# Performance work log

Measured on AMD Instinct MI355X. Metric: run time of the kernel, lower is better.

The kernel has to match this reference:

```python
import jax, jax.numpy as jnp
import numpy as np

B = 1_000_000  # batch size
A = 40         # number of CelebA face attributes
GAMMA = 2.0
EPS = 1e-12


def setup_inputs() -> dict:
    key = jax.random.key(0)
    k1, k2, k3 = jax.random.split(key, 3)
    inputs = jax.random.uniform(k1, (B, A), dtype=jnp.float32)  # probabilities
    targets = jax.random.randint(k2, (A, B), 0, 2, dtype=jnp.int32)  # binary labels, attr-first layout
    attr_loss_weight = jax.random.uniform(k3, (A,), dtype=jnp.float32) + 0.5  # positive per-attr weights
    return {"inputs": inputs, "targets": targets, "attr_loss_weight": attr_loss_weight}


def reference(inputs, targets, attr_loss_weight):
    # inputs: [B, A] probabilities; targets: [A, B] binary labels
    t = targets.T.astype(inputs.dtype)                      # [B, A]
    p = jnp.clip(inputs, EPS, 1.0 - EPS)
    bce = -(t * jnp.log(p) + (1.0 - t) * jnp.log1p(-p))     # elementwise BCE
    w = attr_loss_weight[None, :] * jnp.power(1.0 - inputs, GAMMA)  # focal weight
    # per-sample mean over attributes (F.binary_cross_entropy default), summed over batch
    loss = jnp.sum(jnp.mean(w * bce, axis=1))
    return loss
```

## Files before the change

kernel.cpp:

```cpp
#include <hip/hip_runtime.h>

#define NB 1000000
#define NA 40
#define THREADS 256
#define WPB (THREADS / 64)
#define NBLOCKS 2048
#define NCHUNKS (NB / 64)
#define NEG_LN2_OVER_A (-0.017328679513998632f)

__global__ __launch_bounds__(THREADS) void focal_loss_kernel(
    const float* __restrict__ inputs,
    const int*   __restrict__ targets,
    const float* __restrict__ attr_w,
    float* __restrict__ out)
{
    __shared__ float s_red[WPB];
    const int lane = threadIdx.x & 63;
    const int wid  = blockIdx.x * WPB + (threadIdx.x >> 6);
    const int W    = NBLOCKS * WPB;

    int cj[5], rj[5];
    float4 wt[5];
    #pragma unroll
    for (int j = 0; j < 5; ++j) {
        const int f = lane + 64 * j;
        cj[j] = f / 10;
        rj[j] = 4 * (f - 10 * cj[j]);
        wt[j] = *(const float4*)(attr_w + rj[j]);
    }

    float acc = 0.0f;

    for (int ch = wid; ch < NCHUNKS; ch += W) {
        const int s0 = ch * 64;

        int lab[NA];
        #pragma unroll
        for (int a = 0; a < NA; ++a)
            lab[a] = targets[(size_t)a * NB + (s0 + lane)];

        const float4* in4 = (const float4*)inputs + (size_t)s0 * 10;
        float4 xv[10];
        #pragma unroll
        for (int j = 0; j < 10; ++j)
            xv[j] = in4[lane + 64 * j];

        unsigned wlo = 0u, whi = 0u;
        #pragma unroll
        for (int a = 0; a < 32; ++a) wlo |= (unsigned)(lab[a] & 1) << a;
        #pragma unroll
        for (int a = 32; a < NA; ++a) whi |= (unsigned)(lab[a] & 1) << (a - 32);

#define ELEM(X, BIT, AWK) {                                   \
            const float x_  = (X);                            \
            const float om_ = 1.0f - x_;                      \
            const float w_  = (AWK) * (om_ * om_);            \
            const float p_  = fmaxf(x_,  1e-12f);             \
            const float q_  = fmaxf(om_, 1e-12f);             \
            acc = fmaf(w_, __log2f((BIT) ? p_ : q_), acc); }

        #pragma unroll
        for (int j = 0; j < 10; ++j) {
            const int jj = (j < 5) ? j : j - 5;
            const int cs = cj[jj] + ((j < 5) ? 0 : 32);
            const unsigned lo = (unsigned)__shfl((int)wlo, cs, 64);
            const unsigned hi = (unsigned)__shfl((int)whi, cs, 64);
            const int r = rj[jj];
            const unsigned nib = ((r < 32) ? (lo >> r) : (hi >> (r - 32))) & 15u;
            const float4 x4 = xv[j];
            const float4 w4 = wt[jj];
            ELEM(x4.x, nib & 1u, w4.x)
            ELEM(x4.y, nib & 2u, w4.y)
            ELEM(x4.z, nib & 4u, w4.z)
            ELEM(x4.w, nib & 8u, w4.w)
        }
#undef ELEM
    }

    float v = acc * NEG_LN2_OVER_A;
    #pragma unroll
    for (int off = 32; off > 0; off >>= 1)
        v += __shfl_xor(v, off, 64);
    const int t = threadIdx.x;
    if ((t & 63) == 0) s_red[t >> 6] = v;
    __syncthreads();
    if (t == 0) {
        float r2 = 0.0f;
        #pragma unroll
        for (int w2 = 0; w2 < WPB; ++w2) r2 += s_red[w2];
        atomicAdd(out, r2);
    }
}

extern "C" void kernel_launch(void* const* d_in, const int* in_sizes, int n_in,
                              void* d_out, int out_size, void* d_ws, size_t ws_size,
                              hipStream_t stream) {
    const float* inputs  = (const float*)d_in[0];
    const int*   targets = (const int*)d_in[1];
    const float* attr_w  = (const float*)d_in[2];
    float* out = (float*)d_out;
    hipMemsetAsync(out, 0, sizeof(float), stream);
    focal_loss_kernel<<<dim3(NBLOCKS), dim3(THREADS), 0, stream>>>(inputs, targets, attr_w, out);
}
```

Baseline: 325.4 us.

## Halve chunk size and pack label bits with wave ballots

Each wave now handles 32 samples instead of 64. Targets are loaded as 20 coalesced rows covering two attributes per load, and per-attribute bitmasks are built with __ballot, replacing 40 per-lane label registers and manual bit packing. Per-attribute weights and label bits are fetched with lane shuffles per element, and the launch bound asks for 8 blocks per CU to raise occupancy. The cost is roughly 40 extra shuffles per chunk and half-width row reads of the targets array.

```diff
diff --git a/kernel.cpp b/kernel.cpp
--- a/kernel.cpp
+++ b/kernel.cpp
@@ -5,10 +5,11 @@
 #define THREADS 256
 #define WPB (THREADS / 64)
 #define NBLOCKS 2048
-#define NCHUNKS (NB / 64)
+#define CHUNK 32
+#define NCHUNKS (NB / CHUNK)
 #define NEG_LN2_OVER_A (-0.017328679513998632f)
 
-__global__ __launch_bounds__(THREADS) void focal_loss_kernel(
+__global__ __launch_bounds__(THREADS, 8) void focal_loss_kernel(
     const float* __restrict__ inputs,
     const int*   __restrict__ targets,
     const float* __restrict__ attr_w,
@@ -19,65 +20,59 @@
     const int wid  = blockIdx.x * WPB + (threadIdx.x >> 6);
     const int W    = NBLOCKS * WPB;
 
-    int cj[5], rj[5];
-    float4 wt[5];
+    float awl = 0.0f;
+    if (lane < NA) awl = attr_w[lane] * NEG_LN2_OVER_A;
+
+    int rj[5], sj[5];
     #pragma unroll
     for (int j = 0; j < 5; ++j) {
         const int f = lane + 64 * j;
-        cj[j] = f / 10;
-        rj[j] = 4 * (f - 10 * cj[j]);
-        wt[j] = *(const float4*)(attr_w + rj[j]);
+        const int s = f / 10;
+        rj[j] = 4 * (f - 10 * s);
+        sj[j] = s;
     }
 
     float acc = 0.0f;
 
     for (int ch = wid; ch < NCHUNKS; ch += W) {
-        const int s0 = ch * 64;
-
-        int lab[NA];
-        #pragma unroll
-        for (int a = 0; a < NA; ++a)
-            lab[a] = targets[(size_t)a * NB + (s0 + lane)];
+        const int s0 = ch * CHUNK;
 
         const float4* in4 = (const float4*)inputs + (size_t)s0 * 10;
-        float4 xv[10];
+        float4 xv[5];
         #pragma unroll
-        for (int j = 0; j < 10; ++j)
-            xv[j] = in4[lane + 64 * j];
+        for (int j = 0; j < 5; ++j) xv[j] = in4[lane + 64 * j];
 
-        unsigned wlo = 0u, whi = 0u;
+        unsigned Wbits = 0u;
         #pragma unroll
-        for (int a = 0; a < 32; ++a) wlo |= (unsigned)(lab[a] & 1) << a;
-        #pragma unroll
-        for (int a = 32; a < NA; ++a) whi |= (unsigned)(lab[a] & 1) << (a - 32);
-
-#define ELEM(X, BIT, AWK) {                                   \
-            const float x_  = (X);                            \
-            const float om_ = 1.0f - x_;                      \
-            const float w_  = (AWK) * (om_ * om_);            \
-            const float p_  = fmaxf(x_,  1e-12f);             \
-            const float q_  = fmaxf(om_, 1e-12f);             \
-            acc = fmaf(w_, __log2f((BIT) ? p_ : q_), acc); }
+        for (int k = 0; k < 20; ++k) {
+            const int a  = 2 * k + (lane >> 5);
+            const int tv = targets[(size_t)a * NB + (s0 + (lane & 31))];
+            const unsigned long long m = __ballot(tv != 0);
+            Wbits = (lane == 2 * k)     ? (unsigned)m         : Wbits;
+            Wbits = (lane == 2 * k + 1) ? (unsigned)(m >> 32) : Wbits;
+        }
 
         #pragma unroll
-        for (int j = 0; j < 10; ++j) {
-            const int jj = (j < 5) ? j : j - 5;
-            const int cs = cj[jj] + ((j < 5) ? 0 : 32);
-            const unsigned lo = (unsigned)__shfl((int)wlo, cs, 64);
-            const unsigned hi = (unsigned)__shfl((int)whi, cs, 64);
-            const int r = rj[jj];
-            const unsigned nib = ((r < 32) ? (lo >> r) : (hi >> (r - 32))) & 15u;
-            const float4 x4 = xv[j];
-            const float4 w4 = wt[jj];
-            ELEM(x4.x, nib & 1u, w4.x)
-            ELEM(x4.y, nib & 2u, w4.y)
-            ELEM(x4.z, nib & 4u, w4.z)
-            ELEM(x4.w, nib & 8u, w4.w)
+        for (int j = 0; j < 5; ++j) {
+            const int r  = rj[j];
+            const int si = sj[j];
+            const float xs[4] = {xv[j].x, xv[j].y, xv[j].z, xv[j].w};
+            #pragma unroll
+            for (int c = 0; c < 4; ++c) {
+                const int a = r + c;
+                const unsigned Wa = (unsigned)__shfl((int)Wbits, a, 64);
+                const float wgt   = __shfl(awl, a, 64);
+                const float x_  = xs[c];
+                const float om_ = 1.0f - x_;
+                const float w_  = wgt * (om_ * om_);
+                const float p_  = fmaxf(x_,  1e-12f);
+                const float q_  = fmaxf(om_, 1e-12f);
+                acc = fmaf(w_, __log2f(((Wa >> si) & 1u) ? p_ : q_), acc);
+            }
         }
-#undef ELEM
     }
 
-    float v = acc * NEG_LN2_OVER_A;
+    float v = acc;
     #pragma unroll
     for (int off = 32; off > 0; off >>= 1)
         v += __shfl_xor(v, off, 64);
```

Result: slower. 344.2 us (+5.8%).
